# Performance work log

Measured on AMD Instinct MI355X. Metric: run time of the kernel, lower is better.

Reference implementation:

```python
import jax, jax.numpy as jnp
import numpy as np

N_LAYERS = 2
D_MODEL = 256
N_STATE = 16


def _rmsnorm(x):
    eps = jnp.finfo(x.dtype).eps
    return x * jax.lax.rsqrt(jnp.mean(x * x, axis=-1, keepdims=True) + eps)


def _selective_scan(x, A, W_delta, b_delta, W_B, W_C, D_skip):
    # x: [B, L, D]; A: [D, N] (negative diagonal); W_delta: [D, D]; W_B/W_C: [D, N]
    dt = jax.nn.softplus(jnp.einsum('bld,de->ble', x, W_delta) + b_delta)  # [B,L,D]
    Bm = jnp.einsum('bld,dn->bln', x, W_B)  # [B,L,N]
    Cm = jnp.einsum('bld,dn->bln', x, W_C)  # [B,L,N]
    # ZOH-style discretization: h_t = a_t * h_{t-1} + b_t
    a = jnp.exp(dt[..., None] * A)                              # [B,L,D,N]
    b = dt[..., None] * Bm[:, :, None, :] * x[..., None]        # [B,L,D,N]

    def combine(c1, c2):
        a1, b1 = c1
        a2, b2 = c2
        return a1 * a2, a2 * b1 + b2

    _, h = jax.lax.associative_scan(combine, (a, b), axis=1)    # [B,L,D,N]
    y = jnp.einsum('bldn,bln->bld', h, Cm) + D_skip * x
    return y


def setup_inputs() -> dict:
    key = jax.random.key(0)
    ks = jax.random.split(key, 9)
    B, L, D, N, NL = 2, 4096, D_MODEL, N_STATE, N_LAYERS
    x = jax.random.normal(ks[0], (B, L, D), dtype=jnp.float32)
    # negative real diagonal A (real_random=False baseline init, kept strictly negative)
    A = -(jax.random.uniform(ks[1], (NL, D, N), dtype=jnp.float32) + 0.5)
    sd = 1.0 / np.sqrt(D)
    W_delta = jax.random.normal(ks[2], (NL, D, D), dtype=jnp.float32) * sd
    b_delta = jnp.zeros((NL, D), dtype=jnp.float32)
    W_B = jax.random.normal(ks[3], (NL, D, N), dtype=jnp.float32) * sd
    W_C = jax.random.normal(ks[4], (NL, D, N), dtype=jnp.float32) * sd
    D_skip = jnp.ones((NL, D), dtype=jnp.float32)
    W_mix = jax.random.normal(ks[5], (NL, D, D), dtype=jnp.float32) * sd
    b_mix = jnp.zeros((NL, D), dtype=jnp.float32)
    return {"x": x, "A": A, "W_delta": W_delta, "b_delta": b_delta,
            "W_B": W_B, "W_C": W_C, "D_skip": D_skip,
            "W_mix": W_mix, "b_mix": b_mix}


def reference(x, A, W_delta, b_delta, W_B, W_C, D_skip, W_mix, b_mix):
    h = x
    for l in range(N_LAYERS):
        h = _rmsnorm(h)                                        # RMSNorm (no affine)
        h = _selective_scan(h, A[l], W_delta[l], b_delta[l],
                            W_B[l], W_C[l], D_skip[l])         # S6Block
        h = jax.nn.gelu(h)                                     # activation
        h = jnp.einsum('bld,de->ble', h, W_mix[l]) + b_mix[l]  # MixingBlock
    return _rmsnorm(h)                                          # final RMSNorm
```

## Files before the change

kernel.cpp:

```cpp
#include <hip/hip_runtime.h>
#include <hip/hip_bf16.h>

#define BATCH 2
#define LSEQ 4096
#define DM 256
#define NS 16
#define BL (BATCH*LSEQ)
#define CHUNK 32
#define NCHUNK (LSEQ/CHUNK)
#define NCHAIN (BATCH*DM*NS)
#define SEG 8
#define CPS (NCHUNK/SEG)
#define MS_STRIDE 260
#define LOG2E 1.4426950408889634f

typedef _Float16 f16x8 __attribute__((ext_vector_type(8)));
typedef _Float16 f16x4 __attribute__((ext_vector_type(4)));
typedef float f32x4 __attribute__((ext_vector_type(4)));

__device__ __forceinline__ float softplus_f(float z){
    return fmaxf(z, 0.0f) + log1pf(__expf(-fabsf(z)));
}
__device__ __forceinline__ float gelu_f(float x){
    float u = 0.7978845608028654f*(x + 0.044715f*x*x*x);
    float e = __builtin_amdgcn_exp2f(2.0f*LOG2E*u);
    float th = 1.0f - 2.0f*__builtin_amdgcn_rcpf(e + 1.0f);
    return 0.5f*x*(1.0f + th);
}

__global__ __launch_bounds__(256) void pack_w_k(const float* __restrict__ Wd,
                         const float* __restrict__ WB,
                         const float* __restrict__ WC,
                         const float* __restrict__ Wm,
                         _Float16* __restrict__ pd0, _Float16* __restrict__ pm0,
                         _Float16* __restrict__ pd1, _Float16* __restrict__ pm1){
    int cfg = blockIdx.y;
    int layer = cfg >> 1;
    int isMix = cfg & 1;
    int count = isMix ? 16*8*64 : 18*8*64;
    int t = blockIdx.x*256 + threadIdx.x;
    if (t >= count) return;
    int lane = t & 63;
    int ks   = (t >> 6) & 7;
    int nt16 = t >> 9;
    int col  = nt16*16 + (lane & 15);
    int kb   = ks*32 + ((lane >> 4) << 3);
    const float* Wd_l = Wd + (size_t)layer*DM*DM;
    const float* WB_l = WB + (size_t)layer*DM*NS;
    const float* WC_l = WC + (size_t)layer*DM*NS;
    const float* Wm_l = Wm + (size_t)layer*DM*DM;
    f16x8 v;
    #pragma unroll
    for (int i=0;i<8;++i){
        float s;
        if (isMix)          s = Wm_l[(size_t)(kb+i)*DM + col];
        else if (col < 256) s = Wd_l[(size_t)(kb+i)*DM + col];
        else if (col < 272) s = WB_l[(size_t)(kb+i)*NS + (col-256)];
        else                s = WC_l[(size_t)(kb+i)*NS + (col-272)];
        v[i] = (_Float16)s;
    }
    _Float16* dst = isMix ? (layer ? pm1 : pm0) : (layer ? pd1 : pd0);
    ((f16x8*)dst)[t] = v;
}

__global__ __launch_bounds__(576) void fused_pre(const float* __restrict__ xin,
                          const _Float16* __restrict__ wp,
                          const float* __restrict__ bd,
                          float* __restrict__ xn,
                          float* __restrict__ dt,
                          float* __restrict__ Bm,
                          float* __restrict__ Cm){
    __shared__ _Float16 xs[32*32*8];
    int t = threadIdx.x;
    int row0 = blockIdx.x*32;
    if (t < 512){
        int r = t >> 4;
        int cb = t & 15;
        const float4* src = (const float4*)(xin + (size_t)(row0+r)*DM);
        float4 v[4];
        float ss = 0.0f;
        #pragma unroll
        for (int j=0;j<4;++j){
            v[j] = src[cb + 16*j];
            ss += v[j].x*v[j].x + v[j].y*v[j].y + v[j].z*v[j].z + v[j].w*v[j].w;
        }
        ss += __shfl_xor(ss, 1, 64);
        ss += __shfl_xor(ss, 2, 64);
        ss += __shfl_xor(ss, 4, 64);
        ss += __shfl_xor(ss, 8, 64);
        float s = rsqrtf(ss*(1.0f/DM) + 1.1920929e-07f);
        float4* xout = (float4*)(xn + (size_t)(row0+r)*DM);
        #pragma unroll
        for (int j=0;j<4;++j){
            int c4 = cb + 16*j;
            float4 o; o.x=v[j].x*s; o.y=v[j].y*s; o.z=v[j].z*s; o.w=v[j].w*s;
            xout[c4] = o;
            int slot = c4 >> 1;
            int j0   = (c4 & 1)*4;
            f16x4 hv; hv[0]=(_Float16)o.x; hv[1]=(_Float16)o.y;
            hv[2]=(_Float16)o.z; hv[3]=(_Float16)o.w;
            *(f16x4*)&xs[((size_t)r*32 + (slot ^ (r & 7)))*8 + j0] = hv;
        }
    }
    __syncthreads();
    int w    = t >> 6;
    int lane = t & 63;
    const f16x8* wpb = (const f16x8*)wp;
    int rl = lane & 15;
    int kg = lane >> 4;
    f32x4 acc[2][2] = {};
    #pragma unroll
    for (int ks=0; ks<8; ++ks){
        int s0 = kg + ks*4;
        f16x8 a0 = *(const f16x8*)&xs[((size_t)(rl     )*32 + (s0 ^ (rl & 7)))*8];
        f16x8 a1 = *(const f16x8*)&xs[((size_t)(rl + 16)*32 + (s0 ^ (rl & 7)))*8];
        f16x8 b0 = wpb[((w*2    )*8 + ks)*64 + lane];
        f16x8 b1 = wpb[((w*2 + 1)*8 + ks)*64 + lane];
        acc[0][0] = __builtin_amdgcn_mfma_f32_16x16x32_f16(a0,b0,acc[0][0],0,0,0);
        acc[0][1] = __builtin_amdgcn_mfma_f32_16x16x32_f16(a0,b1,acc[0][1],0,0,0);
        acc[1][0] = __builtin_amdgcn_mfma_f32_16x16x32_f16(a1,b0,acc[1][0],0,0,0);
        acc[1][1] = __builtin_amdgcn_mfma_f32_16x16x32_f16(a1,b1,acc[1][1],0,0,0);
    }
    int c0 = w*32 + (lane & 15);
    int rb = row0 + ((lane >> 4) << 2);
    if (w < 8){
        float bias0 = bd[c0], bias1 = bd[c0 + 16];
        #pragma unroll
        for (int mi=0; mi<2; ++mi){
            #pragma unroll
            for (int r=0; r<4; ++r){
                int grow = rb + mi*16 + r;
                dt[(size_t)grow*DM + c0]      = softplus_f(acc[mi][0][r] + bias0);
                dt[(size_t)grow*DM + c0 + 16] = softplus_f(acc[mi][1][r] + bias1);
            }
        }
    } else {
        int n = lane & 15;
        #pragma unroll
        for (int mi=0; mi<2; ++mi){
            #pragma unroll
            for (int r=0; r<4; ++r){
                int grow = rb + mi*16 + r;
                Bm[(size_t)grow*NS + n] = acc[mi][0][r];
                Cm[(size_t)grow*NS + n] = acc[mi][1][r];
            }
        }
    }
}

__global__ __launch_bounds__(576) void fused_mid(const _Float16* __restrict__ yh,
                          const _Float16* __restrict__ wpm,
                          const float* __restrict__ bm,
                          const _Float16* __restrict__ wpd,
                          const float* __restrict__ bd,
                          float* __restrict__ xn,
                          float* __restrict__ dt,
                          float* __restrict__ Bm,
                          float* __restrict__ Cm){
    __shared__ float ms[32*MS_STRIDE];
    __shared__ _Float16 xs[32*32*8];
    int t = threadIdx.x;
    int w = t >> 6, lane = t & 63;
    int row0 = blockIdx.x*32;
    if (w < 8){
        const f16x8* ah  = (const f16x8*)yh;
        const f16x8* wpb = (const f16x8*)wpm;
        size_t a0i = (size_t)(row0 + (lane & 15))*32 + (lane >> 4);
        f32x4 acc[2][2] = {};
        #pragma unroll
        for (int ks=0; ks<8; ++ks){
            f16x8 a0 = ah[a0i + ks*4];
            f16x8 a1 = ah[a0i + 512 + ks*4];
            f16x8 b0 = wpb[((w*2    )*8 + ks)*64 + lane];
            f16x8 b1 = wpb[((w*2 + 1)*8 + ks)*64 + lane];
            acc[0][0] = __builtin_amdgcn_mfma_f32_16x16x32_f16(a0,b0,acc[0][0],0,0,0);
            acc[0][1] = __builtin_amdgcn_mfma_f32_16x16x32_f16(a0,b1,acc[0][1],0,0,0);
            acc[1][0] = __builtin_amdgcn_mfma_f32_16x16x32_f16(a1,b0,acc[1][0],0,0,0);
            acc[1][1] = __builtin_amdgcn_mfma_f32_16x16x32_f16(a1,b1,acc[1][1],0,0,0);
        }
        int c0 = w*32 + (lane & 15);
        int rb = (lane >> 4) << 2;
        float bias0 = bm[c0], bias1 = bm[c0 + 16];
        #pragma unroll
        for (int mi=0; mi<2; ++mi){
            #pragma unroll
            for (int r=0; r<4; ++r){
                int lr = rb + mi*16 + r;
                ms[lr*MS_STRIDE + c0]      = acc[mi][0][r] + bias0;
                ms[lr*MS_STRIDE + c0 + 16] = acc[mi][1][r] + bias1;
            }
        }
    }
    __syncthreads();
    if (t < 512){
        int r = t >> 4;
        int cb = t & 15;
        float4 v[4];
        float ss = 0.0f;
        #pragma unroll
        for (int j=0;j<4;++j){
            v[j] = *(const float4*)&ms[r*MS_STRIDE + (cb + 16*j)*4];
            ss += v[j].x*v[j].x + v[j].y*v[j].y + v[j].z*v[j].z + v[j].w*v[j].w;
        }
        ss += __shfl_xor(ss, 1, 64);
        ss += __shfl_xor(ss, 2, 64);
        ss += __shfl_xor(ss, 4, 64);
        ss += __shfl_xor(ss, 8, 64);
        float s = rsqrtf(ss*(1.0f/DM) + 1.1920929e-07f);
        float4* xout = (float4*)(xn + (size_t)(row0+r)*DM);
        #pragma unroll
        for (int j=0;j<4;++j){
            int c4 = cb + 16*j;
            float4 o; o.x=v[j].x*s; o.y=v[j].y*s; o.z=v[j].z*s; o.w=v[j].w*s;
            xout[c4] = o;
            int slot = c4 >> 1;
            int j0   = (c4 & 1)*4;
            f16x4 hv; hv[0]=(_Float16)o.x; hv[1]=(_Float16)o.y;
            hv[2]=(_Float16)o.z; hv[3]=(_Float16)o.w;
            *(f16x4*)&xs[((size_t)r*32 + (slot ^ (r & 7)))*8 + j0] = hv;
        }
    }
    __syncthreads();
    {
        const f16x8* wpb = (const f16x8*)wpd;
        int rl = lane & 15;
        int kg = lane >> 4;
        f32x4 acc[2][2] = {};
        #pragma unroll
        for (int ks=0; ks<8; ++ks){
            int s0 = kg + ks*4;
            f16x8 a0 = *(const f16x8*)&xs[((size_t)(rl     )*32 + (s0 ^ (rl & 7)))*8];
            f16x8 a1 = *(const f16x8*)&xs[((size_t)(rl + 16)*32 + (s0 ^ (rl & 7)))*8];
            f16x8 b0 = wpb[((w*2    )*8 + ks)*64 + lane];
            f16x8 b1 = wpb[((w*2 + 1)*8 + ks)*64 + lane];
            acc[0][0] = __builtin_amdgcn_mfma_f32_16x16x32_f16(a0,b0,acc[0][0],0,0,0);
            acc[0][1] = __builtin_amdgcn_mfma_f32_16x16x32_f16(a0,b1,acc[0][1],0,0,0);
            acc[1][0] = __builtin_amdgcn_mfma_f32_16x16x32_f16(a1,b0,acc[1][0],0,0,0);
            acc[1][1] = __builtin_amdgcn_mfma_f32_16x16x32_f16(a1,b1,acc[1][1],0,0,0);
        }
        int c0 = w*32 + (lane & 15);
        int rb = row0 + ((lane >> 4) << 2);
        if (w < 8){
            float bias0 = bd[c0], bias1 = bd[c0 + 16];
            #pragma unroll
            for (int mi=0; mi<2; ++mi){
                #pragma unroll
                for (int r=0; r<4; ++r){
                    int grow = rb + mi*16 + r;
                    dt[(size_t)grow*DM + c0]      = softplus_f(acc[mi][0][r] + bias0);
                    dt[(size_t)grow*DM + c0 + 16] = softplus_f(acc[mi][1][r] + bias1);
                }
            }
        } else {
            int n = lane & 15;
            #pragma unroll
            for (int mi=0; mi<2; ++mi){
                #pragma unroll
                for (int r=0; r<4; ++r){
                    int grow = rb + mi*16 + r;
                    Bm[(size_t)grow*NS + n] = acc[mi][0][r];
                    Cm[(size_t)grow*NS + n] = acc[mi][1][r];
                }
            }
        }
    }
}

__global__ __launch_bounds__(512) void fused_out(const _Float16* __restrict__ yh,
                          const _Float16* __restrict__ wpm,
                          const float* __restrict__ bm,
                          float* __restrict__ out){
    __shared__ float ms[32*MS_STRIDE];
    int t = threadIdx.x;
    int w = t >> 6, lane = t & 63;
    int row0 = blockIdx.x*32;
    {
        const f16x8* ah  = (const f16x8*)yh;
        const f16x8* wpb = (const f16x8*)wpm;
        size_t a0i = (size_t)(row0 + (lane & 15))*32 + (lane >> 4);
        f32x4 acc[2][2] = {};
        #pragma unroll
        for (int ks=0; ks<8; ++ks){
            f16x8 a0 = ah[a0i + ks*4];
            f16x8 a1 = ah[a0i + 512 + ks*4];
            f16x8 b0 = wpb[((w*2    )*8 + ks)*64 + lane];
            f16x8 b1 = wpb[((w*2 + 1)*8 + ks)*64 + lane];
            acc[0][0] = __builtin_amdgcn_mfma_f32_16x16x32_f16(a0,b0,acc[0][0],0,0,0);
            acc[0][1] = __builtin_amdgcn_mfma_f32_16x16x32_f16(a0,b1,acc[0][1],0,0,0);
            acc[1][0] = __builtin_amdgcn_mfma_f32_16x16x32_f16(a1,b0,acc[1][0],0,0,0);
            acc[1][1] = __builtin_amdgcn_mfma_f32_16x16x32_f16(a1,b1,acc[1][1],0,0,0);
        }
        int c0 = w*32 + (lane & 15);
        int rb = (lane >> 4) << 2;
        float bias0 = bm[c0], bias1 = bm[c0 + 16];
        #pragma unroll
        for (int mi=0; mi<2; ++mi){
            #pragma unroll
            for (int r=0; r<4; ++r){
                int lr = rb + mi*16 + r;
                ms[lr*MS_STRIDE + c0]      = acc[mi][0][r] + bias0;
                ms[lr*MS_STRIDE + c0 + 16] = acc[mi][1][r] + bias1;
            }
        }
    }
    __syncthreads();
    {
        int r = t >> 4;
        int cb = t & 15;
        float4 v[4];
        float ss = 0.0f;
        #pragma unroll
        for (int j=0;j<4;++j){
            v[j] = *(const float4*)&ms[r*MS_STRIDE + (cb + 16*j)*4];
            ss += v[j].x*v[j].x + v[j].y*v[j].y + v[j].z*v[j].z + v[j].w*v[j].w;
        }
        ss += __shfl_xor(ss, 1, 64);
        ss += __shfl_xor(ss, 2, 64);
        ss += __shfl_xor(ss, 4, 64);
        ss += __shfl_xor(ss, 8, 64);
        float s = rsqrtf(ss*(1.0f/DM) + 1.1920929e-07f);
        float4* xout = (float4*)(out + (size_t)(row0+r)*DM);
        #pragma unroll
        for (int j=0;j<4;++j){
            float4 o = v[j];
            o.x*=s; o.y*=s; o.z*=s; o.w*=s;
            xout[cb + 16*j] = o;
        }
    }
}

__global__ __launch_bounds__(256) void scan_p1(const float* __restrict__ xn,
                        const float* __restrict__ dt,
                        const float* __restrict__ Bmv,
                        const float* __restrict__ A,
                        float* __restrict__ cA, float* __restrict__ cB){
    __shared__ float4 bs[CHUNK*4];
    int tid = threadIdx.x;
    int c = blockIdx.x, dq = blockIdx.y, b = blockIdx.z;
    int dl = tid >> 2, nq = tid & 3;
    int d  = dq*64 + dl;
    int row0 = b*LSEQ + c*CHUNK;
    if (tid < CHUNK*4) bs[tid] = ((const float4*)(Bmv + (size_t)row0*NS))[tid];
    float4 Alg = ((const float4*)(A + (size_t)d*NS))[nq];
    Alg.x *= LOG2E; Alg.y *= LOG2E; Alg.z *= LOG2E; Alg.w *= LOG2E;
    __syncthreads();
    float Ap0=1,Ap1=1,Ap2=1,Ap3=1, Bp0=0,Bp1=0,Bp2=0,Bp3=0;
    #pragma unroll 4
    for (int tt=0; tt<CHUNK; ++tt){
        float dtv = dt[(size_t)(row0+tt)*DM + d];
        float xv  = xn[(size_t)(row0+tt)*DM + d];
        float dtx = dtv*xv;
        float4 bq = bs[tt*4 + nq];
        float a0 = __builtin_amdgcn_exp2f(dtv*Alg.x);
        float a1 = __builtin_amdgcn_exp2f(dtv*Alg.y);
        float a2 = __builtin_amdgcn_exp2f(dtv*Alg.z);
        float a3 = __builtin_amdgcn_exp2f(dtv*Alg.w);
        Ap0 *= a0; Bp0 = fmaf(a0, Bp0, dtx*bq.x);
        Ap1 *= a1; Bp1 = fmaf(a1, Bp1, dtx*bq.y);
        Ap2 *= a2; Bp2 = fmaf(a2, Bp2, dtx*bq.z);
        Ap3 *= a3; Bp3 = fmaf(a3, Bp3, dtx*bq.w);
    }
    size_t base = (size_t)c*NCHAIN + ((size_t)b*DM + d)*NS + nq*4;
    *(float4*)(cA + base) = make_float4(Ap0,Ap1,Ap2,Ap3);
    *(float4*)(cB + base) = make_float4(Bp0,Bp1,Bp2,Bp3);
}

__global__ __launch_bounds__(256) void scan_p2(const float* __restrict__ cA,
                        const float* __restrict__ cB,
                        float* __restrict__ hin){
    int gt = blockIdx.x*256 + threadIdx.x;
    int chain = gt >> 3;
    int seg   = gt & 7;
    int c0 = seg*CPS;
    float Ac = 1.0f, Bc = 0.0f;
    #pragma unroll 4
    for (int i=0;i<CPS;++i){
        size_t idx = (size_t)(c0+i)*NCHAIN + chain;
        float a = cA[idx], b = cB[idx];
        Bc = fmaf(a, Bc, b);
        Ac *= a;
    }
    #pragma unroll
    for (int dlt=1; dlt<8; dlt<<=1){
        float Apv = __shfl_up(Ac, dlt, 64);
        float Bpv = __shfl_up(Bc, dlt, 64);
        if (seg >= dlt){
            Bc = fmaf(Ac, Bpv, Bc);
            Ac *= Apv;
        }
    }
    float hprev = __shfl_up(Bc, 1, 64);
    float h = (seg == 0) ? 0.0f : hprev;
    #pragma unroll 4
    for (int i=0;i<CPS;++i){
        size_t idx = (size_t)(c0+i)*NCHAIN + chain;
        hin[idx] = h;
        h = fmaf(cA[idx], h, cB[idx]);
    }
}

__global__ __launch_bounds__(256) void scan_p3(const float* __restrict__ xn,
                        const float* __restrict__ dt,
                        const float* __restrict__ Bmv,
                        const float* __restrict__ Cmv,
                        const float* __restrict__ A,
                        const float* __restrict__ Dsk,
                        const float* __restrict__ hin,
                        _Float16* __restrict__ yh){
    __shared__ float4 bs[CHUNK*4], cs[CHUNK*4];
    int tid = threadIdx.x;
    int c = blockIdx.x, dq = blockIdx.y, b = blockIdx.z;
    int dl = tid >> 2, nq = tid & 3;
    int d  = dq*64 + dl;
    int row0 = b*LSEQ + c*CHUNK;
    if (tid < CHUNK*4){
        bs[tid] = ((const float4*)(Bmv + (size_t)row0*NS))[tid];
        cs[tid] = ((const float4*)(Cmv + (size_t)row0*NS))[tid];
    }
    float4 Alg = ((const float4*)(A + (size_t)d*NS))[nq];
    Alg.x *= LOG2E; Alg.y *= LOG2E; Alg.z *= LOG2E; Alg.w *= LOG2E;
    float dsk = Dsk[d];
    float4 hv = ((const float4*)(hin + (size_t)c*NCHAIN + ((size_t)b*DM + d)*NS))[nq];
    float h0=hv.x, h1=hv.y, h2=hv.z, h3=hv.w;
    __syncthreads();
    #pragma unroll 4
    for (int tt=0; tt<CHUNK; ++tt){
        float dtv = dt[(size_t)(row0+tt)*DM + d];
        float xv  = xn[(size_t)(row0+tt)*DM + d];
        float dtx = dtv*xv;
        float4 bq = bs[tt*4 + nq];
        float4 cq = cs[tt*4 + nq];
        float a0 = __builtin_amdgcn_exp2f(dtv*Alg.x);
        float a1 = __builtin_amdgcn_exp2f(dtv*Alg.y);
        float a2 = __builtin_amdgcn_exp2f(dtv*Alg.z);
        float a3 = __builtin_amdgcn_exp2f(dtv*Alg.w);
        h0 = fmaf(a0, h0, dtx*bq.x);
        h1 = fmaf(a1, h1, dtx*bq.y);
        h2 = fmaf(a2, h2, dtx*bq.z);
        h3 = fmaf(a3, h3, dtx*bq.w);
        float p = fmaf(h0, cq.x, fmaf(h1, cq.y, fmaf(h2, cq.z, h3*cq.w)));
        p += __shfl_xor(p, 1, 64);
        p += __shfl_xor(p, 2, 64);
        if (nq == 0){
            float yv = p + dsk*xv;
            yh[(size_t)(row0+tt)*DM + d] = (_Float16)gelu_f(yv);
        }
    }
}

extern "C" void kernel_launch(void* const* d_in, const int* in_sizes, int n_in,
                              void* d_out, int out_size, void* d_ws, size_t ws_size,
                              hipStream_t stream) {
    const float* x  = (const float*)d_in[0];
    const float* A  = (const float*)d_in[1];
    const float* Wd = (const float*)d_in[2];
    const float* bd = (const float*)d_in[3];
    const float* WB = (const float*)d_in[4];
    const float* WC = (const float*)d_in[5];
    const float* Ds = (const float*)d_in[6];
    const float* Wm = (const float*)d_in[7];
    const float* bm = (const float*)d_in[8];
    float* out = (float*)d_out;

    const size_t BSZ = (size_t)BL*DM;
    const size_t CH  = (size_t)NCHUNK*NCHAIN;
    float* ws  = (float*)d_ws;
    float* b0  = ws;
    float* b1  = b0  + BSZ;
    float* b2  = b1  + BSZ;
    float* Bmb = b2  + BSZ;
    float* Cmb = Bmb + (size_t)BL*NS;
    float* cA  = Cmb + (size_t)BL*NS;
    float* cB  = cA  + CH;
    float* hin = cB  + CH;
    _Float16* packs = (_Float16*)(hin + CH);
    _Float16* pd0 = packs;
    _Float16* pd1 = pd0 + 73728;
    _Float16* pm0 = pd1 + 73728;
    _Float16* pm1 = pm0 + 65536;
    _Float16* yh = (_Float16*)cB;

    dim3 gscan(NCHUNK, DM/64, BATCH);

    pack_w_k<<<dim3(36,4), 256, 0, stream>>>(Wd, WB, WC, Wm, pd0, pm0, pd1, pm1);

    const float* A1  = A  + (size_t)DM*NS;
    const float* bd1 = bd + DM;
    const float* Ds1 = Ds + DM;
    const float* bm1 = bm + DM;

    fused_pre<<<BL/32, 576, 0, stream>>>(x, pd0, bd, b0, b1, Bmb, Cmb);
    scan_p1<<<gscan, 256, 0, stream>>>(b0, b1, Bmb, A, cA, cB);
    scan_p2<<<NCHAIN*SEG/256, 256, 0, stream>>>(cA, cB, hin);
    scan_p3<<<gscan, 256, 0, stream>>>(b0, b1, Bmb, Cmb, A, Ds, hin, yh);
    fused_mid<<<BL/32, 576, 0, stream>>>(yh, pm0, bm, pd1, bd1, b0, b1, Bmb, Cmb);
    scan_p1<<<gscan, 256, 0, stream>>>(b0, b1, Bmb, A1, cA, cB);
    scan_p2<<<NCHAIN*SEG/256, 256, 0, stream>>>(cA, cB, hin);
    scan_p3<<<gscan, 256, 0, stream>>>(b0, b1, Bmb, Cmb, A1, Ds1, hin, yh);
    fused_out<<<BL/32, 512, 0, stream>>>(yh, pm1, bm1, out);
}
```

Baseline: 182.4 us.

## Replace three-pass chunked scan with single-pass decoupled look-back scan

Merges the chunk-aggregate, cross-chunk prefix and output passes of the selective scan into one kernel. Each block publishes its chunk aggregate and, later, its inclusive prefix through flagged global slots. Later blocks walk back over those slots to get their carry-in. dt and x are staged once in shared memory and reused by both sweeps, which removes two launches and the round trips through cA/cB/hin per layer. The risks are spin-wait stalls if blocks are not scheduled in chunk order, plus an extra memset and packed 64-bit atomic traffic.

```diff
diff --git a/kernel.cpp b/kernel.cpp
--- a/kernel.cpp
+++ b/kernel.cpp
@@ -8,15 +8,14 @@
 #define BL (BATCH*LSEQ)
 #define CHUNK 32
 #define NCHUNK (LSEQ/CHUNK)
-#define NCHAIN (BATCH*DM*NS)
-#define SEG 8
-#define CPS (NCHUNK/SEG)
+#define NSEQ (4*BATCH)
 #define MS_STRIDE 260
 #define LOG2E 1.4426950408889634f
 
 typedef _Float16 f16x8 __attribute__((ext_vector_type(8)));
 typedef _Float16 f16x4 __attribute__((ext_vector_type(4)));
 typedef float f32x4 __attribute__((ext_vector_type(4)));
+typedef unsigned long long ull;
 
 __device__ __forceinline__ float softplus_f(float z){
     return fmaxf(z, 0.0f) + log1pf(__expf(-fabsf(z)));
@@ -26,6 +25,9 @@
     float e = __builtin_amdgcn_exp2f(2.0f*LOG2E*u);
     float th = 1.0f - 2.0f*__builtin_amdgcn_rcpf(e + 1.0f);
     return 0.5f*x*(1.0f + th);
+}
+__device__ __forceinline__ ull pack_ab(float a, float b){
+    return ((ull)__float_as_uint(b) << 32) | (ull)__float_as_uint(a);
 }
 
 __global__ __launch_bounds__(256) void pack_w_k(const float* __restrict__ Wd,
@@ -329,116 +331,127 @@
     }
 }
 
-__global__ __launch_bounds__(256) void scan_p1(const float* __restrict__ xn,
-                        const float* __restrict__ dt,
-                        const float* __restrict__ Bmv,
-                        const float* __restrict__ A,
-                        float* __restrict__ cA, float* __restrict__ cB){
-    __shared__ float4 bs[CHUNK*4];
-    int tid = threadIdx.x;
-    int c = blockIdx.x, dq = blockIdx.y, b = blockIdx.z;
-    int dl = tid >> 2, nq = tid & 3;
-    int d  = dq*64 + dl;
-    int row0 = b*LSEQ + c*CHUNK;
-    if (tid < CHUNK*4) bs[tid] = ((const float4*)(Bmv + (size_t)row0*NS))[tid];
-    float4 Alg = ((const float4*)(A + (size_t)d*NS))[nq];
-    Alg.x *= LOG2E; Alg.y *= LOG2E; Alg.z *= LOG2E; Alg.w *= LOG2E;
-    __syncthreads();
-    float Ap0=1,Ap1=1,Ap2=1,Ap3=1, Bp0=0,Bp1=0,Bp2=0,Bp3=0;
-    #pragma unroll 4
-    for (int tt=0; tt<CHUNK; ++tt){
-        float dtv = dt[(size_t)(row0+tt)*DM + d];
-        float xv  = xn[(size_t)(row0+tt)*DM + d];
-        float dtx = dtv*xv;
-        float4 bq = bs[tt*4 + nq];
-        float a0 = __builtin_amdgcn_exp2f(dtv*Alg.x);
-        float a1 = __builtin_amdgcn_exp2f(dtv*Alg.y);
-        float a2 = __builtin_amdgcn_exp2f(dtv*Alg.z);
-        float a3 = __builtin_amdgcn_exp2f(dtv*Alg.w);
-        Ap0 *= a0; Bp0 = fmaf(a0, Bp0, dtx*bq.x);
-        Ap1 *= a1; Bp1 = fmaf(a1, Bp1, dtx*bq.y);
-        Ap2 *= a2; Bp2 = fmaf(a2, Bp2, dtx*bq.z);
-        Ap3 *= a3; Bp3 = fmaf(a3, Bp3, dtx*bq.w);
-    }
-    size_t base = (size_t)c*NCHAIN + ((size_t)b*DM + d)*NS + nq*4;
-    *(float4*)(cA + base) = make_float4(Ap0,Ap1,Ap2,Ap3);
-    *(float4*)(cB + base) = make_float4(Bp0,Bp1,Bp2,Bp3);
-}
-
-__global__ __launch_bounds__(256) void scan_p2(const float* __restrict__ cA,
-                        const float* __restrict__ cB,
-                        float* __restrict__ hin){
-    int gt = blockIdx.x*256 + threadIdx.x;
-    int chain = gt >> 3;
-    int seg   = gt & 7;
-    int c0 = seg*CPS;
-    float Ac = 1.0f, Bc = 0.0f;
-    #pragma unroll 4
-    for (int i=0;i<CPS;++i){
-        size_t idx = (size_t)(c0+i)*NCHAIN + chain;
-        float a = cA[idx], b = cB[idx];
-        Bc = fmaf(a, Bc, b);
-        Ac *= a;
-    }
-    #pragma unroll
-    for (int dlt=1; dlt<8; dlt<<=1){
-        float Apv = __shfl_up(Ac, dlt, 64);
-        float Bpv = __shfl_up(Bc, dlt, 64);
-        if (seg >= dlt){
-            Bc = fmaf(Ac, Bpv, Bc);
-            Ac *= Apv;
-        }
-    }
-    float hprev = __shfl_up(Bc, 1, 64);
-    float h = (seg == 0) ? 0.0f : hprev;
-    #pragma unroll 4
-    for (int i=0;i<CPS;++i){
-        size_t idx = (size_t)(c0+i)*NCHAIN + chain;
-        hin[idx] = h;
-        h = fmaf(cA[idx], h, cB[idx]);
-    }
-}
-
-__global__ __launch_bounds__(256) void scan_p3(const float* __restrict__ xn,
+__global__ __launch_bounds__(256) void scan_lb(const float* __restrict__ xn,
                         const float* __restrict__ dt,
                         const float* __restrict__ Bmv,
                         const float* __restrict__ Cmv,
                         const float* __restrict__ A,
                         const float* __restrict__ Dsk,
-                        const float* __restrict__ hin,
-                        _Float16* __restrict__ yh){
+                        ull* __restrict__ agg,
+                        ull* __restrict__ incl,
+                        int* __restrict__ flags,
+                        _Float16* __restrict__ yh,
+                        int genA, int genI){
+    __shared__ float sdt[CHUNK][64];
+    __shared__ float sxn[CHUNK][64];
     __shared__ float4 bs[CHUNK*4], cs[CHUNK*4];
+    __shared__ int relay;
     int tid = threadIdx.x;
     int c = blockIdx.x, dq = blockIdx.y, b = blockIdx.z;
+    int seq = dq + 4*b;
     int dl = tid >> 2, nq = tid & 3;
     int d  = dq*64 + dl;
     int row0 = b*LSEQ + c*CHUNK;
+    {
+        int fi = tid;
+        int t0 = fi >> 4, cg = fi & 15;
+        *(float4*)&sdt[t0][cg*4]    = *(const float4*)(dt + (size_t)(row0+t0)*DM + dq*64 + cg*4);
+        *(float4*)&sxn[t0][cg*4]    = *(const float4*)(xn + (size_t)(row0+t0)*DM + dq*64 + cg*4);
+        int t1 = t0 + 16;
+        *(float4*)&sdt[t1][cg*4]    = *(const float4*)(dt + (size_t)(row0+t1)*DM + dq*64 + cg*4);
+        *(float4*)&sxn[t1][cg*4]    = *(const float4*)(xn + (size_t)(row0+t1)*DM + dq*64 + cg*4);
+    }
     if (tid < CHUNK*4){
         bs[tid] = ((const float4*)(Bmv + (size_t)row0*NS))[tid];
         cs[tid] = ((const float4*)(Cmv + (size_t)row0*NS))[tid];
     }
     float4 Alg = ((const float4*)(A + (size_t)d*NS))[nq];
-    Alg.x *= LOG2E; Alg.y *= LOG2E; Alg.z *= LOG2E; Alg.w *= LOG2E;
+    float alg[4] = {Alg.x*LOG2E, Alg.y*LOG2E, Alg.z*LOG2E, Alg.w*LOG2E};
     float dsk = Dsk[d];
-    float4 hv = ((const float4*)(hin + (size_t)c*NCHAIN + ((size_t)b*DM + d)*NS))[nq];
-    float h0=hv.x, h1=hv.y, h2=hv.z, h3=hv.w;
-    __syncthreads();
+    __syncthreads();
+    float Ap[4] = {1,1,1,1}, Bp[4] = {0,0,0,0};
     #pragma unroll 4
     for (int tt=0; tt<CHUNK; ++tt){
-        float dtv = dt[(size_t)(row0+tt)*DM + d];
-        float xv  = xn[(size_t)(row0+tt)*DM + d];
+        float dtv = sdt[tt][dl];
+        float xv  = sxn[tt][dl];
+        float dtx = dtv*xv;
+        float4 bq = bs[tt*4 + nq];
+        float bv[4] = {bq.x, bq.y, bq.z, bq.w};
+        #pragma unroll
+        for (int j=0;j<4;++j){
+            float a = __builtin_amdgcn_exp2f(dtv*alg[j]);
+            Ap[j] *= a;
+            Bp[j] = fmaf(a, Bp[j], dtx*bv[j]);
+        }
+    }
+    size_t base = ((size_t)(seq*NCHUNK + c))*1024 + (size_t)dl*16 + nq*4;
+    #pragma unroll
+    for (int j=0;j<4;++j)
+        __hip_atomic_store(&agg[base+j], pack_ab(Ap[j], Bp[j]),
+                           __ATOMIC_RELAXED, __HIP_MEMORY_SCOPE_AGENT);
+    __syncthreads();
+    if (tid == 0)
+        __hip_atomic_store(&flags[seq*NCHUNK + c], genA,
+                           __ATOMIC_RELEASE, __HIP_MEMORY_SCOPE_AGENT);
+    float Ae[4] = {1,1,1,1}, Be[4] = {0,0,0,0};
+    int k = c - 1;
+    while (k >= 0){
+        __syncthreads();
+        if (tid == 0){
+            int f;
+            do {
+                f = __hip_atomic_load(&flags[seq*NCHUNK + k],
+                                      __ATOMIC_RELAXED, __HIP_MEMORY_SCOPE_AGENT);
+                if (f != genA && f != genI) __builtin_amdgcn_s_sleep(2);
+            } while (f != genA && f != genI);
+            (void)__hip_atomic_load(&flags[seq*NCHUNK + k],
+                                    __ATOMIC_ACQUIRE, __HIP_MEMORY_SCOPE_AGENT);
+            relay = f;
+        }
+        __syncthreads();
+        int f = relay;
+        const ull* src = (f == genI) ? incl : agg;
+        size_t kb = ((size_t)(seq*NCHUNK + k))*1024 + (size_t)dl*16 + nq*4;
+        #pragma unroll
+        for (int j=0;j<4;++j){
+            ull wv = __hip_atomic_load(&src[kb+j],
+                                       __ATOMIC_RELAXED, __HIP_MEMORY_SCOPE_AGENT);
+            float Ak = __uint_as_float((unsigned)wv);
+            float Bk = __uint_as_float((unsigned)(wv >> 32));
+            Be[j] = fmaf(Ae[j], Bk, Be[j]);
+            Ae[j] *= Ak;
+        }
+        if (f == genI) break;
+        --k;
+    }
+    #pragma unroll
+    for (int j=0;j<4;++j){
+        float Ai = Ap[j]*Ae[j];
+        float Bi = fmaf(Ap[j], Be[j], Bp[j]);
+        __hip_atomic_store(&incl[base+j], pack_ab(Ai, Bi),
+                           __ATOMIC_RELAXED, __HIP_MEMORY_SCOPE_AGENT);
+    }
+    __syncthreads();
+    if (tid == 0)
+        __hip_atomic_store(&flags[seq*NCHUNK + c], genI,
+                           __ATOMIC_RELEASE, __HIP_MEMORY_SCOPE_AGENT);
+    float h[4] = {Be[0], Be[1], Be[2], Be[3]};
+    #pragma unroll 4
+    for (int tt=0; tt<CHUNK; ++tt){
+        float dtv = sdt[tt][dl];
+        float xv  = sxn[tt][dl];
         float dtx = dtv*xv;
         float4 bq = bs[tt*4 + nq];
         float4 cq = cs[tt*4 + nq];
-        float a0 = __builtin_amdgcn_exp2f(dtv*Alg.x);
-        float a1 = __builtin_amdgcn_exp2f(dtv*Alg.y);
-        float a2 = __builtin_amdgcn_exp2f(dtv*Alg.z);
-        float a3 = __builtin_amdgcn_exp2f(dtv*Alg.w);
-        h0 = fmaf(a0, h0, dtx*bq.x);
-        h1 = fmaf(a1, h1, dtx*bq.y);
-        h2 = fmaf(a2, h2, dtx*bq.z);
-        h3 = fmaf(a3, h3, dtx*bq.w);
-        float p = fmaf(h0, cq.x, fmaf(h1, cq.y, fmaf(h2, cq.z, h3*cq.w)));
+        float bv[4] = {bq.x, bq.y, bq.z, bq.w};
+        float cv[4] = {cq.x, cq.y, cq.z, cq.w};
+        float p = 0.0f;
+        #pragma unroll
+        for (int j=0;j<4;++j){
+            float a = __builtin_amdgcn_exp2f(dtv*alg[j]);
+            h[j] = fmaf(a, h[j], dtx*bv[j]);
+            p = fmaf(h[j], cv[j], p);
+        }
         p += __shfl_xor(p, 1, 64);
         p += __shfl_xor(p, 2, 64);
         if (nq == 0){
@@ -463,25 +476,25 @@
     float* out = (float*)d_out;
 
     const size_t BSZ = (size_t)BL*DM;
-    const size_t CH  = (size_t)NCHUNK*NCHAIN;
+    const size_t CHW = (size_t)NSEQ*NCHUNK*1024;
     float* ws  = (float*)d_ws;
     float* b0  = ws;
     float* b1  = b0  + BSZ;
-    float* b2  = b1  + BSZ;
-    float* Bmb = b2  + BSZ;
+    float* Bmb = b1  + BSZ;
     float* Cmb = Bmb + (size_t)BL*NS;
-    float* cA  = Cmb + (size_t)BL*NS;
-    float* cB  = cA  + CH;
-    float* hin = cB  + CH;
-    _Float16* packs = (_Float16*)(hin + CH);
+    ull*  aggb = (ull*)(Cmb + (size_t)BL*NS);
+    ull*  incb = aggb + CHW;
+    int*  flags = (int*)(incb + CHW);
+    _Float16* packs = (_Float16*)(flags + 1024);
     _Float16* pd0 = packs;
     _Float16* pd1 = pd0 + 73728;
     _Float16* pm0 = pd1 + 73728;
     _Float16* pm1 = pm0 + 65536;
-    _Float16* yh = (_Float16*)cB;
+    _Float16* yh  = pm1 + 65536;
 
     dim3 gscan(NCHUNK, DM/64, BATCH);
 
+    hipMemsetAsync(flags, 0, NSEQ*NCHUNK*sizeof(int), stream);
     pack_w_k<<<dim3(36,4), 256, 0, stream>>>(Wd, WB, WC, Wm, pd0, pm0, pd1, pm1);
 
     const float* A1  = A  + (size_t)DM*NS;
@@ -490,12 +503,10 @@
     const float* bm1 = bm + DM;
 
     fused_pre<<<BL/32, 576, 0, stream>>>(x, pd0, bd, b0, b1, Bmb, Cmb);
-    scan_p1<<<gscan, 256, 0, stream>>>(b0, b1, Bmb, A, cA, cB);
-    scan_p2<<<NCHAIN*SEG/256, 256, 0, stream>>>(cA, cB, hin);
-    scan_p3<<<gscan, 256, 0, stream>>>(b0, b1, Bmb, Cmb, A, Ds, hin, yh);
+    scan_lb<<<gscan, 256, 0, stream>>>(b0, b1, Bmb, Cmb, A, Ds,
+                                       aggb, incb, flags, yh, 1, 2);
     fused_mid<<<BL/32, 576, 0, stream>>>(yh, pm0, bm, pd1, bd1, b0, b1, Bmb, Cmb);
-    scan_p1<<<gscan, 256, 0, stream>>>(b0, b1, Bmb, A1, cA, cB);
-    scan_p2<<<NCHAIN*SEG/256, 256, 0, stream>>>(cA, cB, hin);
-    scan_p3<<<gscan, 256, 0, stream>>>(b0, b1, Bmb, Cmb, A1, Ds1, hin, yh);
+    scan_lb<<<gscan, 256, 0, stream>>>(b0, b1, Bmb, Cmb, A1, Ds1,
+                                       aggb, incb, flags, yh, 3, 4);
     fused_out<<<BL/32, 512, 0, stream>>>(yh, pm1, bm1, out);
 }
```

Result: slower. 495.5 us (+171.7%).

## Fold chunk-carry scan into scan_p3 and stage dt/x tiles in LDS

Applied to the files above, without the earlier changes.

Removes the scan_p2 kernel. Each scan_p3 block now rebuilds its incoming state by walking the per-chunk (A,B) summaries of all earlier chunks serially, which saves one launch per layer and the hin buffer. scan_p1 and scan_p3 also load the dt and xn tiles into shared memory with coalesced float4 loads, replacing strided scalar global reads. The cost is that later chunks do O(c) prefix work, up to 127 float4 load pairs per thread, so total redundant reads grow quadratically with the chunk count.

```diff
diff --git a/kernel.cpp b/kernel.cpp
--- a/kernel.cpp
+++ b/kernel.cpp
@@ -9,8 +9,6 @@
 #define CHUNK 32
 #define NCHUNK (LSEQ/CHUNK)
 #define NCHAIN (BATCH*DM*NS)
-#define SEG 8
-#define CPS (NCHUNK/SEG)
 #define MS_STRIDE 260
 #define LOG2E 1.4426950408889634f
 
@@ -334,12 +332,22 @@
                         const float* __restrict__ Bmv,
                         const float* __restrict__ A,
                         float* __restrict__ cA, float* __restrict__ cB){
+    __shared__ float sdt[CHUNK][64];
+    __shared__ float sxn[CHUNK][64];
     __shared__ float4 bs[CHUNK*4];
     int tid = threadIdx.x;
     int c = blockIdx.x, dq = blockIdx.y, b = blockIdx.z;
     int dl = tid >> 2, nq = tid & 3;
     int d  = dq*64 + dl;
     int row0 = b*LSEQ + c*CHUNK;
+    {
+        int t0 = tid >> 4, cg = tid & 15;
+        *(float4*)&sdt[t0][cg*4] = *(const float4*)(dt + (size_t)(row0+t0)*DM + dq*64 + cg*4);
+        *(float4*)&sxn[t0][cg*4] = *(const float4*)(xn + (size_t)(row0+t0)*DM + dq*64 + cg*4);
+        int t1 = t0 + 16;
+        *(float4*)&sdt[t1][cg*4] = *(const float4*)(dt + (size_t)(row0+t1)*DM + dq*64 + cg*4);
+        *(float4*)&sxn[t1][cg*4] = *(const float4*)(xn + (size_t)(row0+t1)*DM + dq*64 + cg*4);
+    }
     if (tid < CHUNK*4) bs[tid] = ((const float4*)(Bmv + (size_t)row0*NS))[tid];
     float4 Alg = ((const float4*)(A + (size_t)d*NS))[nq];
     Alg.x *= LOG2E; Alg.y *= LOG2E; Alg.z *= LOG2E; Alg.w *= LOG2E;
@@ -347,8 +355,8 @@
     float Ap0=1,Ap1=1,Ap2=1,Ap3=1, Bp0=0,Bp1=0,Bp2=0,Bp3=0;
     #pragma unroll 4
     for (int tt=0; tt<CHUNK; ++tt){
-        float dtv = dt[(size_t)(row0+tt)*DM + d];
-        float xv  = xn[(size_t)(row0+tt)*DM + d];
+        float dtv = sdt[tt][dl];
+        float xv  = sxn[tt][dl];
         float dtx = dtv*xv;
         float4 bq = bs[tt*4 + nq];
         float a0 = __builtin_amdgcn_exp2f(dtv*Alg.x);
@@ -365,54 +373,31 @@
     *(float4*)(cB + base) = make_float4(Bp0,Bp1,Bp2,Bp3);
 }
 
-__global__ __launch_bounds__(256) void scan_p2(const float* __restrict__ cA,
-                        const float* __restrict__ cB,
-                        float* __restrict__ hin){
-    int gt = blockIdx.x*256 + threadIdx.x;
-    int chain = gt >> 3;
-    int seg   = gt & 7;
-    int c0 = seg*CPS;
-    float Ac = 1.0f, Bc = 0.0f;
-    #pragma unroll 4
-    for (int i=0;i<CPS;++i){
-        size_t idx = (size_t)(c0+i)*NCHAIN + chain;
-        float a = cA[idx], b = cB[idx];
-        Bc = fmaf(a, Bc, b);
-        Ac *= a;
-    }
-    #pragma unroll
-    for (int dlt=1; dlt<8; dlt<<=1){
-        float Apv = __shfl_up(Ac, dlt, 64);
-        float Bpv = __shfl_up(Bc, dlt, 64);
-        if (seg >= dlt){
-            Bc = fmaf(Ac, Bpv, Bc);
-            Ac *= Apv;
-        }
-    }
-    float hprev = __shfl_up(Bc, 1, 64);
-    float h = (seg == 0) ? 0.0f : hprev;
-    #pragma unroll 4
-    for (int i=0;i<CPS;++i){
-        size_t idx = (size_t)(c0+i)*NCHAIN + chain;
-        hin[idx] = h;
-        h = fmaf(cA[idx], h, cB[idx]);
-    }
-}
-
 __global__ __launch_bounds__(256) void scan_p3(const float* __restrict__ xn,
                         const float* __restrict__ dt,
                         const float* __restrict__ Bmv,
                         const float* __restrict__ Cmv,
                         const float* __restrict__ A,
                         const float* __restrict__ Dsk,
-                        const float* __restrict__ hin,
+                        const float* __restrict__ cA,
+                        const float* __restrict__ cB,
                         _Float16* __restrict__ yh){
+    __shared__ float sdt[CHUNK][64];
+    __shared__ float sxn[CHUNK][64];
     __shared__ float4 bs[CHUNK*4], cs[CHUNK*4];
     int tid = threadIdx.x;
     int c = blockIdx.x, dq = blockIdx.y, b = blockIdx.z;
     int dl = tid >> 2, nq = tid & 3;
     int d  = dq*64 + dl;
     int row0 = b*LSEQ + c*CHUNK;
+    {
+        int t0 = tid >> 4, cg = tid & 15;
+        *(float4*)&sdt[t0][cg*4] = *(const float4*)(dt + (size_t)(row0+t0)*DM + dq*64 + cg*4);
+        *(float4*)&sxn[t0][cg*4] = *(const float4*)(xn + (size_t)(row0+t0)*DM + dq*64 + cg*4);
+        int t1 = t0 + 16;
+        *(float4*)&sdt[t1][cg*4] = *(const float4*)(dt + (size_t)(row0+t1)*DM + dq*64 + cg*4);
+        *(float4*)&sxn[t1][cg*4] = *(const float4*)(xn + (size_t)(row0+t1)*DM + dq*64 + cg*4);
+    }
     if (tid < CHUNK*4){
         bs[tid] = ((const float4*)(Bmv + (size_t)row0*NS))[tid];
         cs[tid] = ((const float4*)(Cmv + (size_t)row0*NS))[tid];
@@ -420,13 +405,22 @@
     float4 Alg = ((const float4*)(A + (size_t)d*NS))[nq];
     Alg.x *= LOG2E; Alg.y *= LOG2E; Alg.z *= LOG2E; Alg.w *= LOG2E;
     float dsk = Dsk[d];
-    float4 hv = ((const float4*)(hin + (size_t)c*NCHAIN + ((size_t)b*DM + d)*NS))[nq];
-    float h0=hv.x, h1=hv.y, h2=hv.z, h3=hv.w;
+    float h0=0.0f, h1=0.0f, h2=0.0f, h3=0.0f;
+    size_t cbase = ((size_t)b*DM + d)*NS + nq*4;
+    #pragma unroll 4
+    for (int k=0; k<c; ++k){
+        float4 av = *(const float4*)(cA + (size_t)k*NCHAIN + cbase);
+        float4 bv = *(const float4*)(cB + (size_t)k*NCHAIN + cbase);
+        h0 = fmaf(av.x, h0, bv.x);
+        h1 = fmaf(av.y, h1, bv.y);
+        h2 = fmaf(av.z, h2, bv.z);
+        h3 = fmaf(av.w, h3, bv.w);
+    }
     __syncthreads();
     #pragma unroll 4
     for (int tt=0; tt<CHUNK; ++tt){
-        float dtv = dt[(size_t)(row0+tt)*DM + d];
-        float xv  = xn[(size_t)(row0+tt)*DM + d];
+        float dtv = sdt[tt][dl];
+        float xv  = sxn[tt][dl];
         float dtx = dtv*xv;
         float4 bq = bs[tt*4 + nq];
         float4 cq = cs[tt*4 + nq];
@@ -467,18 +461,16 @@
     float* ws  = (float*)d_ws;
     float* b0  = ws;
     float* b1  = b0  + BSZ;
-    float* b2  = b1  + BSZ;
-    float* Bmb = b2  + BSZ;
+    float* Bmb = b1  + BSZ;
     float* Cmb = Bmb + (size_t)BL*NS;
     float* cA  = Cmb + (size_t)BL*NS;
     float* cB  = cA  + CH;
-    float* hin = cB  + CH;
-    _Float16* packs = (_Float16*)(hin + CH);
+    _Float16* packs = (_Float16*)(cB + CH);
     _Float16* pd0 = packs;
     _Float16* pd1 = pd0 + 73728;
     _Float16* pm0 = pd1 + 73728;
     _Float16* pm1 = pm0 + 65536;
-    _Float16* yh = (_Float16*)cB;
+    _Float16* yh  = pm1 + 65536;
 
     dim3 gscan(NCHUNK, DM/64, BATCH);
 
@@ -491,11 +483,9 @@
 
     fused_pre<<<BL/32, 576, 0, stream>>>(x, pd0, bd, b0, b1, Bmb, Cmb);
     scan_p1<<<gscan, 256, 0, stream>>>(b0, b1, Bmb, A, cA, cB);
-    scan_p2<<<NCHAIN*SEG/256, 256, 0, stream>>>(cA, cB, hin);
-    scan_p3<<<gscan, 256, 0, stream>>>(b0, b1, Bmb, Cmb, A, Ds, hin, yh);
+    scan_p3<<<gscan, 256, 0, stream>>>(b0, b1, Bmb, Cmb, A, Ds, cA, cB, yh);
     fused_mid<<<BL/32, 576, 0, stream>>>(yh, pm0, bm, pd1, bd1, b0, b1, Bmb, Cmb);
     scan_p1<<<gscan, 256, 0, stream>>>(b0, b1, Bmb, A1, cA, cB);
-    scan_p2<<<NCHAIN*SEG/256, 256, 0, stream>>>(cA, cB, hin);
-    scan_p3<<<gscan, 256, 0, stream>>>(b0, b1, Bmb, Cmb, A1, Ds1, hin, yh);
+    scan_p3<<<gscan, 256, 0, stream>>>(b0, b1, Bmb, Cmb, A1, Ds1, cA, cB, yh);
     fused_out<<<BL/32, 512, 0, stream>>>(yh, pm1, bm1, out);
 }
```

Measured after the change: 221.0 us. 21.2% more time.
